# Performance work log

Hardware: AMD Instinct MI355X
Metric: run time of the kernel (lower is better)

The kernel has to match this reference:

```python
import jax, jax.numpy as jnp
import numpy as np

N = 50000        # nodes
E = 800000       # edges (avg degree 16)
DIN = 256        # input feature dim
D = 128          # embedding_dim
B = 8            # graphs in batch
ITERS = 2        # num_iterations


def setup_inputs() -> dict:
    key = jax.random.key(0)
    ks = jax.random.split(key, 16)
    w = lambda k, shape: jax.random.normal(k, shape, jnp.float32) * 0.05
    z = lambda n: jnp.zeros((n,), jnp.float32)
    return {
        "nodes": jax.random.normal(ks[0], (N, DIN), jnp.float32),
        "edges": jax.random.randint(ks[1], (2, E), 0, N),
        "batch": jnp.sort(jax.random.randint(ks[2], (N,), 0, B)),
        # initial encoder Linear(DIN, D)
        "W_enc": w(ks[3], (DIN, D)), "b_enc": z(D),
        # parent aggregation MLP: Linear(2D, D) -> ReLU -> Linear(D, D)
        "Wp1": w(ks[4], (2 * D, D)), "bp1": z(D),
        "Wp2": w(ks[5], (D, D)), "bp2": z(D),
        # child aggregation MLP
        "Wc1": w(ks[6], (2 * D, D)), "bc1": z(D),
        "Wc2": w(ks[7], (D, D)), "bc2": z(D),
        # final agg: Linear(3D, 2D) -> ReLU -> Linear(2D, D)
        "Wf1": w(ks[8], (3 * D, 2 * D)), "bf1": z(2 * D),
        "Wf2": w(ks[9], (2 * D, D)), "bf2": z(D),
        # Conv1d(D, 2D, kernel=1) == Linear(D, 2D)
        "Wconv": w(ks[10], (D, 2 * D)), "bconv": z(2 * D),
    }


def _edge_agg(x, idx_i, idx_j, W1, b1, W2, b2, inv_deg):
    # message: mlp(cat(x_i, x_j)); scatter-sum at idx_i; degree-normalize.
    h = jnp.concatenate([x[idx_i], x[idx_j]], axis=1)         # [E, 2D]
    m = jax.nn.relu(h @ W1 + b1) @ W2 + b2                    # [E, D]
    agg = jax.ops.segment_sum(m, idx_i, num_segments=x.shape[0])
    return agg * inv_deg[:, None]


def reference(nodes, edges, batch, W_enc, b_enc, Wp1, bp1, Wp2, bp2,
              Wc1, bc1, Wc2, bc2, Wf1, bf1, Wf2, bf2, Wconv, bconv):
    src, dst = edges[0], edges[1]
    ones_e = jnp.ones((edges.shape[1],), nodes.dtype)
    deg_dst = jax.ops.segment_sum(ones_e, dst, num_segments=N)
    deg_src = jax.ops.segment_sum(ones_e, src, num_segments=N)
    inv_dst = jnp.where(deg_dst > 0, 1.0 / deg_dst, 0.0)
    inv_src = jnp.where(deg_src > 0, 1.0 / deg_src, 0.0)

    x = nodes @ W_enc + b_enc                                  # [N, D]
    for _ in range(ITERS):
        # Parent_Aggregation: x_i = x[dst], x_j = x[src], sum at dst, / in-deg
        fi = _edge_agg(x, dst, src, Wp1, bp1, Wp2, bp2, inv_dst)
        # Child_Aggregation:  x_i = x[src], x_j = x[dst], sum at src, / out-deg
        fo = _edge_agg(x, src, dst, Wc1, bc1, Wc2, bc2, inv_src)
        h = jnp.concatenate([x, fi, fo], axis=1)               # [N, 3D]
        x = x + (jax.nn.relu(h @ Wf1 + bf1) @ Wf2 + bf2)

    y = x @ Wconv + bconv                                      # conv1d k=1 -> [N, 2D]
    gmax = jax.ops.segment_max(y, batch, num_segments=B)       # global_max_pool
    cnt = jax.ops.segment_sum(jnp.ones((N,), y.dtype), batch, num_segments=B)
    gmean = jax.ops.segment_sum(y, batch, num_segments=B) / cnt[:, None]
    return jnp.concatenate([gmax, gmean], axis=1)              # [B, 4D]
```

## Files before the change

### kernel.cpp

```cpp
#include <hip/hip_runtime.h>
#include <hip/hip_bf16.h>
#include <float.h>

typedef __hip_bfloat16 bf16;
typedef short short8 __attribute__((ext_vector_type(8)));
typedef short short4v __attribute__((ext_vector_type(4)));
typedef float f32x4 __attribute__((ext_vector_type(4)));
typedef unsigned short u16;
typedef unsigned char u8;

__device__ __forceinline__ float toF(bf16 v) { return __bfloat162float(v); }
__device__ __forceinline__ float s2f(short s) {
    return __uint_as_float(((unsigned int)(unsigned short)s) << 16);
}
__device__ __forceinline__ short f2s(float f) {
    bf16 h = __float2bfloat16(f);
    return *(short*)&h;
}
__device__ __forceinline__ float rdw(const void* p, int i, int f) {
    return f ? toF(((const bf16*)p)[i]) : ((const float*)p)[i];
}

__global__ void diag_kernel(float* __restrict__ out, float v, int n) {
    int i = blockIdx.x * 256 + threadIdx.x;
    if (i < n) out[i] = v;
}

__global__ void init_kernel(int* __restrict__ deg2, float* __restrict__ cnt_gsum,
                            float* __restrict__ gmax, int* __restrict__ flag, int n2) {
    int i = blockIdx.x * 256 + threadIdx.x;
    if (i < n2) deg2[i] = 0;
    if (i < 8 + 2048) cnt_gsum[i] = 0.f;
    if (i < 2048) gmax[i] = -FLT_MAX;
    if (i == 0) *flag = 1;
}

__global__ void probe_kernel(const unsigned int* __restrict__ w, int nwords,
                             int* __restrict__ flag) {
    int i = blockIdx.x * 256 + threadIdx.x;
    bool bad = false;
    if (i < nwords) {
        float v = __uint_as_float((w[i] & 0xFFFFu) << 16);
        bad = !(v > -1e3f && v < 1e3f);
    }
    if (__any(bad) && (threadIdx.x & 63) == 0) atomicAnd(flag, 0);
}

struct M1 {
    const int* edges; int E;
    int* degd; int* degs; u8* rankd; u8* ranks;
    const int* batch; int Nn; float* cnt;
    const void* wsrc[7]; int woff[7]; bf16* wdst[7];
    int wK[7]; int wNC[7]; int wstart[8];
    const void* bsrc[8]; bf16* bdst[8]; int bn[8];
    const void* nsrc; bf16* ndst; int nElems;
    const void* w2praw; const void* w2craw; const void* wf1raw;
    const void* b2praw; const void* b2craw;
    bf16* wsf1; bf16* ub; bf16* vb;
    const int* flag;
    int sCnt, sSwz, sBias, sConv, sFw, sUv;
};

__global__ void mega1_kernel(M1 a) {
    int b = blockIdx.x, tid = threadIdx.x;
    if (b < a.sCnt) {
        const int* es = a.edges;
        const int* ed = a.edges + a.E;
        int e0 = (b * 256 + tid) * 4;
        if (e0 + 4 <= a.E) {
            int4 s4 = *(const int4*)(es + e0);
            int4 d4 = *(const int4*)(ed + e0);
            uchar4 rs, rd;
            rs.x = (u8)atomicAdd(&a.degs[s4.x], 1);
            rs.y = (u8)atomicAdd(&a.degs[s4.y], 1);
            rs.z = (u8)atomicAdd(&a.degs[s4.z], 1);
            rs.w = (u8)atomicAdd(&a.degs[s4.w], 1);
            rd.x = (u8)atomicAdd(&a.degd[d4.x], 1);
            rd.y = (u8)atomicAdd(&a.degd[d4.y], 1);
            rd.z = (u8)atomicAdd(&a.degd[d4.z], 1);
            rd.w = (u8)atomicAdd(&a.degd[d4.w], 1);
            *(uchar4*)(a.ranks + e0) = rs;
            *(uchar4*)(a.rankd + e0) = rd;
        } else {
            for (int e = e0; e < a.E; ++e) {
                a.ranks[e] = (u8)atomicAdd(&a.degs[es[e]], 1);
                a.rankd[e] = (u8)atomicAdd(&a.degd[ed[e]], 1);
            }
        }
    } else if (b < a.sSwz) {
        __shared__ float loc[8];
        if (tid < 8) loc[tid] = 0.f;
        __syncthreads();
        int i = (b - a.sCnt) * 256 + tid;
        if (i < a.Nn) atomicAdd(&loc[a.batch[i]], 1.0f);
        __syncthreads();
        if (tid < 8 && loc[tid] > 0.f) atomicAdd(&a.cnt[tid], loc[tid]);
    } else if (b < a.sBias) {
        int bb = b - a.sSwz;
        int seg = 0;
#pragma unroll
        for (int t = 1; t < 7; ++t) if (bb >= a.wstart[t]) seg = t;
        int i = (bb - a.wstart[seg]) * 256 + tid;
        int K = a.wK[seg], NC = a.wNC[seg];
        if (i < K * NC) {
            int KF = K >> 5;
            int j = i & 7;
            int ln = (i >> 3) & 63;
            int q = i >> 9;
            int kb = q % KF;
            int t = q / KF;
            int k = kb * 32 + (ln >> 4) * 8 + j;
            int n = t * 16 + (ln & 15);
            int idx = a.woff[seg] + k * NC + n;
            a.wdst[seg][i] = (*a.flag)
                ? ((const bf16*)a.wsrc[seg])[idx]
                : __float2bfloat16(((const float*)a.wsrc[seg])[idx]);
        }
    } else if (b < a.sConv) {
#pragma unroll
        for (int t = 0; t < 8; ++t)
            for (int i = tid; i < a.bn[t]; i += 256)
                a.bdst[t][i] = (*a.flag)
                    ? ((const bf16*)a.bsrc[t])[i]
                    : __float2bfloat16(((const float*)a.bsrc[t])[i]);
    } else if (b < a.sFw) {
        if (*a.flag) return;
        int i = (b - a.sConv) * 2048 + tid * 8;
        if (i + 8 <= a.nElems) {
            const float* f = (const float*)a.nsrc + i;
            short8 o;
#pragma unroll
            for (int j = 0; j < 8; ++j) o[j] = f2s(f[j]);
            *(short8*)((short*)a.ndst + i) = o;
        } else {
            int e = a.nElems;
            for (int jj = i; jj < e && jj < i + 8; ++jj)
                a.ndst[jj] = __float2bfloat16(((const float*)a.nsrc)[jj]);
        }
    } else if (b < a.sUv) {
        int i = (b - a.sFw) * 256 + tid;
        int j = i & 7;
        int ln = (i >> 3) & 63;
        int q = i >> 9;
        int kb = q % 12;
        int t = q / 12;
        int k = kb * 32 + (ln >> 4) * 8 + j;
        int n = t * 16 + (ln & 15);
        int f = *a.flag;
        float val;
        if (k < 128) {
            val = rdw(a.wf1raw, k * 256 + n, f);
        } else {
            const void* w2 = (k < 256) ? a.w2praw : a.w2craw;
            int arow = k & 127;
            int base = (k < 256) ? 128 : 256;
            float s = 0.f;
            for (int c = 0; c < 128; ++c)
                s += rdw(w2, arow * 128 + c, f) * rdw(a.wf1raw, (base + c) * 256 + n, f);
            val = s;
        }
        a.wsf1[i] = __float2bfloat16(val);
    } else {
        if (tid < 256) {
            int f = *a.flag;
            float su = 0.f, sv = 0.f;
            for (int c = 0; c < 128; ++c) {
                su += rdw(a.b2praw, c, f) * rdw(a.wf1raw, (128 + c) * 256 + tid, f);
                sv += rdw(a.b2craw, c, f) * rdw(a.wf1raw, (256 + c) * 256 + tid, f);
            }
            a.ub[tid] = __float2bfloat16(su);
            a.vb[tid] = __float2bfloat16(sv);
        }
    }
}

__device__ __forceinline__ void atomicMaxF(float* addr, float val) {
    unsigned int* ua = (unsigned int*)addr;
    unsigned int old = __float_as_uint(*addr);
    while (__uint_as_float(old) < val) {
        unsigned int assumed = old;
        old = atomicCAS(ua, assumed, __float_as_uint(val));
        if (old == assumed) break;
    }
}

template<int K, int NC> struct SB {
    static constexpr int APAD = K + 8;
    static constexpr int CPAD = NC + 8;
    static constexpr int AB = 64 * APAD * 2;
    static constexpr int CB = 64 * CPAD * 2;
    static constexpr int S = AB > CB ? AB : CB;
};

template<int K, int NC, int NSRC, bool RELU, bool RES, bool POOL, bool STORE>
__device__ __forceinline__ void gemm_core(int bx,
    const bf16* A0, const bf16* A1, const bf16* A2,
    const bf16* WS, const bf16* bias, bf16* C, int M,
    const int* batch, float* gmax, float* gsum, char* smem) {
    constexpr int KF = K / 32;
    constexpr int NH = NC / 128;
    constexpr int APAD = SB<K, NC>::APAD;
    constexpr int CPAD = SB<K, NC>::CPAD;
    short* sA = (short*)smem;

    int tid = threadIdx.x;
    int m0blk = bx * 64;

    constexpr int C8 = K / 8;
    for (int idx = tid; idx < 64 * C8; idx += 256) {
        int r = idx / C8, c8 = idx % C8;
        int row = m0blk + r; row = row < M ? row : M - 1;
        const bf16* src;
        int off;
        if (NSRC == 1) { src = A0; off = c8 * 8; }
        else {
            int seg = c8 >> 4;
            src = seg == 0 ? A0 : (seg == 1 ? A1 : A2);
            off = (c8 & 15) * 8;
        }
        const size_t rs = (NSRC == 1) ? (size_t)K : (size_t)128;
        *(short8*)(sA + r * APAD + c8 * 8) = *(const short8*)((const short*)src + (size_t)row * rs + off);
    }
    __syncthreads();

    int wv = tid >> 6, ln = tid & 63;
    int quad = ln >> 4, ncol = ln & 15;
    int mw = wv * 16;

    short8 a[KF];
#pragma unroll
    for (int kb = 0; kb < KF; ++kb)
        a[kb] = *(const short8*)(sA + (mw + ncol) * APAD + kb * 32 + quad * 8);
    __syncthreads();

    short* sC = (short*)smem;
    const short8* wsp = (const short8*)WS;
#pragma unroll
    for (int h = 0; h < NH; ++h) {
        f32x4 acc[8];
#pragma unroll
        for (int t = 0; t < 8; ++t) acc[t] = (f32x4){0.f, 0.f, 0.f, 0.f};
        short8 bcur[8], bnxt[8];
#pragma unroll
        for (int t = 0; t < 8; ++t)
            bcur[t] = wsp[(size_t)((h * 8 + t) * KF) * 64 + ln];
#pragma unroll
        for (int kb = 0; kb < KF; ++kb) {
            if (kb + 1 < KF) {
#pragma unroll
                for (int t = 0; t < 8; ++t)
                    bnxt[t] = wsp[(size_t)((h * 8 + t) * KF + kb + 1) * 64 + ln];
            }
#pragma unroll
            for (int t = 0; t < 8; ++t)
                acc[t] = __builtin_amdgcn_mfma_f32_16x16x32_bf16(a[kb], bcur[t], acc[t], 0, 0, 0);
#pragma unroll
            for (int t = 0; t < 8; ++t) bcur[t] = bnxt[t];
        }
#pragma unroll
        for (int t = 0; t < 8; ++t) {
            float bv = bias ? toF(bias[h * 128 + t * 16 + ncol]) : 0.f;
#pragma unroll
            for (int r = 0; r < 4; ++r) {
                float v = acc[t][r] + bv;
                if (RELU) v = fmaxf(v, 0.f);
                sC[(mw + quad * 4 + r) * CPAD + h * 128 + t * 16 + ncol] = f2s(v);
            }
        }
    }
    __syncthreads();
    if (!STORE && !POOL) return;

    if (POOL) {
        int* bs = (int*)(smem + SB<K, NC>::S);
        if (tid < 64) {
            int row = m0blk + tid;
            bs[tid] = (row < M) ? batch[row] : -1;
        }
        __syncthreads();
        int cur_b = -1;
        float mx = -FLT_MAX, sm = 0.f;
        for (int r = 0; r < 64; ++r) {
            int b = bs[r];
            if (b < 0) break;
            float v = s2f(sC[r * CPAD + tid]);
            if (b != cur_b) {
                if (cur_b >= 0) {
                    atomicMaxF(&gmax[cur_b * 256 + tid], mx);
                    atomicAdd(&gsum[cur_b * 256 + tid], sm);
                }
                cur_b = b; mx = v; sm = v;
            } else {
                mx = fmaxf(mx, v);
                sm += v;
            }
        }
        if (cur_b >= 0) {
            atomicMaxF(&gmax[cur_b * 256 + tid], mx);
            atomicAdd(&gsum[cur_b * 256 + tid], sm);
        }
    } else {
        constexpr int OC8 = NC / 8;
        for (int idx = tid; idx < 64 * OC8; idx += 256) {
            int r = idx / OC8, c8 = idx % OC8;
            int row = m0blk + r;
            if (row < M) {
                short8 v = *(short8*)(sC + r * CPAD + c8 * 8);
                size_t o = (size_t)row * NC + c8 * 8;
                if (RES) {
                    short8 old = *(const short8*)((const short*)C + o);
#pragma unroll
                    for (int j = 0; j < 8; ++j) v[j] = f2s(s2f(v[j]) + s2f(old[j]));
                }
                *(short8*)((short*)C + o) = v;
            }
        }
    }
}

template<int K, int NC, int NSRC, bool RELU, bool RES, bool POOL>
__global__ __launch_bounds__(256, 2)
void gemm_mfma_kernel(const bf16* A0, const bf16* A1, const bf16* A2,
                      const bf16* WS, const bf16* bias, bf16* C, int M,
                      const int* batch, float* gmax, float* gsum) {
    __shared__ __align__(16) char smem[SB<K, NC>::S + (POOL ? 256 : 0)];
    gemm_core<K, NC, NSRC, RELU, RES, POOL, true>(
        blockIdx.x, A0, A1, A2, WS, bias, C, M, batch, gmax, gsum, smem);
}

__global__ __launch_bounds__(256, 2)
void sei_kernel(const int* __restrict__ edges, int E,
                const u8* __restrict__ rankd, const u8* __restrict__ ranks,
                u16* __restrict__ adjd, u16* __restrict__ adjs, int CAP,
                const void* nodes_raw, const bf16* Tn, const int* flag,
                const bf16* WSenc, const bf16* benc, bf16* x, int M,
                const int* degd, const int* degs,
                float* invd, float* invs, int gsc, int gb) {
    __shared__ __align__(16) char smem[SB<256, 128>::S];
    int b = blockIdx.x, tid = threadIdx.x;
    if (b < gsc) {
        int e0 = (b * 256 + tid) * 4;
        if (e0 + 4 <= E) {
            int4 s4 = *(const int4*)(edges + e0);
            int4 d4 = *(const int4*)(edges + E + e0);
            uchar4 rs = *(const uchar4*)(ranks + e0);
            uchar4 rd = *(const uchar4*)(rankd + e0);
            if (rs.x < CAP) adjs[s4.x * CAP + rs.x] = (u16)d4.x;
            if (rs.y < CAP) adjs[s4.y * CAP + rs.y] = (u16)d4.y;
            if (rs.z < CAP) adjs[s4.z * CAP + rs.z] = (u16)d4.z;
            if (rs.w < CAP) adjs[s4.w * CAP + rs.w] = (u16)d4.w;
            if (rd.x < CAP) adjd[d4.x * CAP + rd.x] = (u16)s4.x;
            if (rd.y < CAP) adjd[d4.y * CAP + rd.y] = (u16)s4.y;
            if (rd.z < CAP) adjd[d4.z * CAP + rd.z] = (u16)s4.z;
            if (rd.w < CAP) adjd[d4.w * CAP + rd.w] = (u16)s4.w;
        } else {
            for (int e = e0; e < E; ++e) {
                int s_ = edges[e], d_ = edges[E + e];
                if (ranks[e] < CAP) adjs[s_ * CAP + ranks[e]] = (u16)d_;
                if (rankd[e] < CAP) adjd[d_ * CAP + rankd[e]] = (u16)s_;
            }
        }
    } else if (b < gsc + gb) {
        const bf16* A0 = (*flag) ? (const bf16*)nodes_raw : Tn;
        gemm_core<256, 128, 1, false, false, false, true>(
            b - gsc, A0, nullptr, nullptr, WSenc, benc, x, M,
            nullptr, nullptr, nullptr, smem);
    } else {
        int i = (b - gsc - gb) * 256 + tid;
        if (i < M) {
            int dd = degd[i]; invd[i] = dd > 0 ? 1.0f / (float)dd : 0.0f;
            int ds = degs[i]; invs[i] = ds > 0 ? 1.0f / (float)ds : 0.0f;
        }
    }
}

__device__ __forceinline__ void agg_body(int node, int tid,
        const int* __restrict__ deg, const u16* __restrict__ adj, int CAP,
        const float* __restrict__ inv,
        const short* __restrict__ PQ, int stride,
        const short* __restrict__ b1, bf16* __restrict__ S) {
    int ln = tid & 63;
    int c4 = ln & 31, half = ln >> 5;
    float p[4];
    {
        short4v pv = *(const short4v*)(PQ + (size_t)node * stride + 4 * c4);
        short4v bv = *(const short4v*)(b1 + 4 * c4);
#pragma unroll
        for (int r = 0; r < 4; ++r) p[r] = s2f(pv[r]) + s2f(bv[r]);
    }
    float a[4] = {0.f, 0.f, 0.f, 0.f};
    int d = deg[node]; d = d < CAP ? d : CAP;
    float invv = inv[node];
    const u16* ap = adj + (size_t)node * CAP;
    const short* Qb = PQ + 128 + 4 * c4;
    int k = half;
    for (; k + 14 < d; k += 16) {
        int j0 = ap[k],      j1 = ap[k + 2],  j2 = ap[k + 4],  j3 = ap[k + 6];
        int j4 = ap[k + 8],  j5 = ap[k + 10], j6 = ap[k + 12], j7 = ap[k + 14];
        short4v q0 = *(const short4v*)(Qb + (size_t)j0 * stride);
        short4v q1 = *(const short4v*)(Qb + (size_t)j1 * stride);
        short4v q2 = *(const short4v*)(Qb + (size_t)j2 * stride);
        short4v q3 = *(const short4v*)(Qb + (size_t)j3 * stride);
        short4v q4 = *(const short4v*)(Qb + (size_t)j4 * stride);
        short4v q5 = *(const short4v*)(Qb + (size_t)j5 * stride);
        short4v q6 = *(const short4v*)(Qb + (size_t)j6 * stride);
        short4v q7 = *(const short4v*)(Qb + (size_t)j7 * stride);
#pragma unroll
        for (int r = 0; r < 4; ++r)
            a[r] += fmaxf(p[r] + s2f(q0[r]), 0.f) + fmaxf(p[r] + s2f(q1[r]), 0.f)
                  + fmaxf(p[r] + s2f(q2[r]), 0.f) + fmaxf(p[r] + s2f(q3[r]), 0.f)
                  + fmaxf(p[r] + s2f(q4[r]), 0.f) + fmaxf(p[r] + s2f(q5[r]), 0.f)
                  + fmaxf(p[r] + s2f(q6[r]), 0.f) + fmaxf(p[r] + s2f(q7[r]), 0.f);
    }
    for (; k + 6 < d; k += 8) {
        int j0 = ap[k], j1 = ap[k + 2], j2 = ap[k + 4], j3 = ap[k + 6];
        short4v q0 = *(const short4v*)(Qb + (size_t)j0 * stride);
        short4v q1 = *(const short4v*)(Qb + (size_t)j1 * stride);
        short4v q2 = *(const short4v*)(Qb + (size_t)j2 * stride);
        short4v q3 = *(const short4v*)(Qb + (size_t)j3 * stride);
#pragma unroll
        for (int r = 0; r < 4; ++r)
            a[r] += fmaxf(p[r] + s2f(q0[r]), 0.f) + fmaxf(p[r] + s2f(q1[r]), 0.f)
                  + fmaxf(p[r] + s2f(q2[r]), 0.f) + fmaxf(p[r] + s2f(q3[r]), 0.f);
    }
    for (; k < d; k += 2) {
        int j = ap[k];
        short4v q = *(const short4v*)(Qb + (size_t)j * stride);
#pragma unroll
        for (int r = 0; r < 4; ++r) a[r] += fmaxf(p[r] + s2f(q[r]), 0.f);
    }
#pragma unroll
    for (int r = 0; r < 4; ++r) a[r] += __shfl_xor(a[r], 32);
    if (half == 0) {
        short4v o;
#pragma unroll
        for (int r = 0; r < 4; ++r) o[r] = f2s(a[r] * invv);
        *(short4v*)((short*)S + (size_t)node * 128 + 4 * c4) = o;
    }
}

__global__ void agg_kernel(const int* deg, const u16* adj, int CAP,
                           const float* inv, const bf16* PQ, int stride,
                           const bf16* b1, bf16* S, int M) {
    int node = blockIdx.x * 4 + (threadIdx.x >> 6);
    if (node >= M) return;
    agg_body(node, threadIdx.x, deg, adj, CAP, inv, (const short*)PQ, stride,
             (const short*)b1, S);
}

__global__ void agg2_kernel(const int* degd, const u16* adjd, const float* invd,
                            const int* degs, const u16* adjs, const float* invs,
                            int CAP, const bf16* T, const bf16* b1p, const bf16* b1c,
                            bf16* Sd, bf16* Ss, int M, int ga) {
    int b = blockIdx.x, wv = threadIdx.x >> 6;
    if (b < ga) {
        int node = b * 4 + wv;
        if (node < M)
            agg_body(node, threadIdx.x, degd, adjd, CAP, invd, (const short*)T, 512,
                     (const short*)b1p, Sd);
    } else {
        int node = (b - ga) * 4 + wv;
        if (node < M)
            agg_body(node, threadIdx.x, degs, adjs, CAP, invs, (const short*)T + 256, 512,
                     (const short*)b1c, Ss);
    }
}

template<bool FINAL>
__global__ __launch_bounds__(256, 2)
void mega_mlp_kernel(const bf16* __restrict__ x, const bf16* Sd, const bf16* Ss,
                     const int* __restrict__ degd, const int* __restrict__ degs,
                     const bf16* __restrict__ ub, const bf16* __restrict__ vb,
                     const bf16* WSf1, const bf16* bf1_,
                     const bf16* WSf2, const bf16* bf2_,
                     bf16* xio, int M,
                     const bf16* WSconv, const bf16* bconv,
                     const int* batch, float* gmax, float* gsum) {
    __shared__ __align__(16) char smem[52224 + 256];
    constexpr int RB = 17408;
    short* sm = (short*)smem;
    int tid = threadIdx.x;
    int m0blk = blockIdx.x * 64;

#pragma unroll
    for (int reg = 0; reg < 3; ++reg) {
        const short* sp = reg == 0 ? (const short*)x
                        : (reg == 1 ? (const short*)Sd : (const short*)Ss);
        for (int idx = tid; idx < 64 * 16; idx += 256) {
            int r = idx >> 4, c8 = idx & 15;
            int row = m0blk + r; row = row < M ? row : M - 1;
            *(short8*)(sm + reg * (RB / 2) + r * 136 + c8 * 8) =
                *(const short8*)(sp + (size_t)row * 128 + c8 * 8);
        }
    }
    __syncthreads();

    int wv = tid >> 6, ln = tid & 63;
    int quad = ln >> 4, ncol = ln & 15;
    int mw = wv * 16;

    short8 a1[12];
#pragma unroll
    for (int kb = 0; kb < 12; ++kb) {
        const short* sb = sm + (kb >> 2) * (RB / 2);
        a1[kb] = *(const short8*)(sb + (mw + ncol) * 136 + (kb & 3) * 32 + quad * 8);
    }
    __syncthreads();

    bool md[4], ms[4];
#pragma unroll
    for (int r = 0; r < 4; ++r) {
        int orow = m0blk + mw + quad * 4 + r; orow = orow < M ? orow : M - 1;
        md[r] = degd[orow] > 0;
        ms[r] = degs[orow] > 0;
    }

    short* sH = sm + RB / 2;
    const short8* w1 = (const short8*)WSf1;
#pragma unroll
    for (int h = 0; h < 2; ++h) {
        f32x4 acc[8];
#pragma unroll
        for (int t = 0; t < 8; ++t) acc[t] = (f32x4){0.f, 0.f, 0.f, 0.f};
        short8 bcur[8], bnxt[8];
#pragma unroll
        for (int t = 0; t < 8; ++t)
            bcur[t] = w1[(size_t)((h * 8 + t) * 12) * 64 + ln];
#pragma unroll
        for (int kb = 0; kb < 12; ++kb) {
            if (kb + 1 < 12) {
#pragma unroll
                for (int t = 0; t < 8; ++t)
                    bnxt[t] = w1[(size_t)((h * 8 + t) * 12 + kb + 1) * 64 + ln];
            }
#pragma unroll
            for (int t = 0; t < 8; ++t)
                acc[t] = __builtin_amdgcn_mfma_f32_16x16x32_bf16(a1[kb], bcur[t], acc[t], 0, 0, 0);
#pragma unroll
            for (int t = 0; t < 8; ++t) bcur[t] = bnxt[t];
        }
#pragma unroll
        for (int t = 0; t < 8; ++t) {
            int col = h * 128 + t * 16 + ncol;
            float bv = toF(bf1_[col]);
            float uu = toF(ub[col]);
            float vv = toF(vb[col]);
#pragma unroll
            for (int r = 0; r < 4; ++r) {
                float v = acc[t][r] + bv + (md[r] ? uu : 0.f) + (ms[r] ? vv : 0.f);
                sH[(mw + quad * 4 + r) * 264 + col] = f2s(fmaxf(v, 0.f));
            }
        }
    }
    __syncthreads();

    short8 a2[8];
#pragma unroll
    for (int kb = 0; kb < 8; ++kb)
        a2[kb] = *(const short8*)(sH + (mw + ncol) * 264 + kb * 32 + quad * 8);
    __syncthreads();

    f32x4 acc2[8];
#pragma unroll
    for (int t = 0; t < 8; ++t) acc2[t] = (f32x4){0.f, 0.f, 0.f, 0.f};
    const short8* w2 = (const short8*)WSf2;
    {
        short8 bcur[8], bnxt[8];
#pragma unroll
        for (int t = 0; t < 8; ++t) bcur[t] = w2[(size_t)(t * 8) * 64 + ln];
#pragma unroll
        for (int kb = 0; kb < 8; ++kb) {
            if (kb + 1 < 8) {
#pragma unroll
                for (int t = 0; t < 8; ++t)
                    bnxt[t] = w2[(size_t)(t * 8 + kb + 1) * 64 + ln];
            }
#pragma unroll
            for (int t = 0; t < 8; ++t)
                acc2[t] = __builtin_amdgcn_mfma_f32_16x16x32_bf16(a2[kb], bcur[t], acc2[t], 0, 0, 0);
#pragma unroll
            for (int t = 0; t < 8; ++t) bcur[t] = bnxt[t];
        }
    }
    short* sC2 = sm + RB / 2;
#pragma unroll
    for (int t = 0; t < 8; ++t) {
        float bv = toF(bf2_[t * 16 + ncol]);
#pragma unroll
        for (int r = 0; r < 4; ++r)
            sC2[(mw + quad * 4 + r) * 136 + t * 16 + ncol] = f2s(acc2[t][r] + bv);
    }
    __syncthreads();

    for (int idx = tid; idx < 64 * 16; idx += 256) {
        int r = idx >> 4, c8 = idx & 15;
        short8 v = *(short8*)(sC2 + r * 136 + c8 * 8);
        short8 old = *(const short8*)(sm + r * 136 + c8 * 8);
#pragma unroll
        for (int j = 0; j < 8; ++j) v[j] = f2s(s2f(v[j]) + s2f(old[j]));
        if (FINAL) {
            *(short8*)(sC2 + r * 136 + c8 * 8) = v;
        } else {
            int row = m0blk + r;
            if (row < M) *(short8*)((short*)xio + (size_t)row * 128 + c8 * 8) = v;
        }
    }
    if (!FINAL) return;
    __syncthreads();

    short8 a3[4];
#pragma unroll
    for (int kb = 0; kb < 4; ++kb)
        a3[kb] = *(const short8*)(sC2 + (mw + ncol) * 136 + kb * 32 + quad * 8);
    __syncthreads();

    short* sCc = sm;
    const short8* wc = (const short8*)WSconv;
#pragma unroll
    for (int h = 0; h < 2; ++h) {
        f32x4 acc[8];
#pragma unroll
        for (int t = 0; t < 8; ++t) acc[t] = (f32x4){0.f, 0.f, 0.f, 0.f};
        short8 bcur[8], bnxt[8];
#pragma unroll
        for (int t = 0; t < 8; ++t)
            bcur[t] = wc[(size_t)((h * 8 + t) * 4) * 64 + ln];
#pragma unroll
        for (int kb = 0; kb < 4; ++kb) {
            if (kb + 1 < 4) {
#pragma unroll
                for (int t = 0; t < 8; ++t)
                    bnxt[t] = wc[(size_t)((h * 8 + t) * 4 + kb + 1) * 64 + ln];
            }
#pragma unroll
            for (int t = 0; t < 8; ++t)
                acc[t] = __builtin_amdgcn_mfma_f32_16x16x32_bf16(a3[kb], bcur[t], acc[t], 0, 0, 0);
#pragma unroll
            for (int t = 0; t < 8; ++t) bcur[t] = bnxt[t];
        }
#pragma unroll
        for (int t = 0; t < 8; ++t) {
            float bv = toF(bconv[h * 128 + t * 16 + ncol]);
#pragma unroll
            for (int r = 0; r < 4; ++r)
                sCc[(mw + quad * 4 + r) * 264 + h * 128 + t * 16 + ncol] =
                    f2s(acc[t][r] + bv);
        }
    }
    __syncthreads();

    int* bs = (int*)(smem + 52224);
    if (tid < 64) {
        int row = m0blk + tid;
        bs[tid] = (row < M) ? batch[row] : -1;
    }
    __syncthreads();
    int cur_b = -1;
    float mx = -FLT_MAX, sum_ = 0.f;
    for (int r = 0; r < 64; ++r) {
        int b = bs[r];
        if (b < 0) break;
        float v = s2f(sCc[r * 264 + tid]);
        if (b != cur_b) {
            if (cur_b >= 0) {
                atomicMaxF(&gmax[cur_b * 256 + tid], mx);
                atomicAdd(&gsum[cur_b * 256 + tid], sum_);
            }
            cur_b = b; mx = v; sum_ = v;
        } else {
            mx = fmaxf(mx, v);
            sum_ += v;
        }
    }
    if (cur_b >= 0) {
        atomicMaxF(&gmax[cur_b * 256 + tid], mx);
        atomicAdd(&gsum[cur_b * 256 + tid], sum_);
    }
}

__global__ void out_kernel(const float* __restrict__ gmax, const float* __restrict__ gsum,
                           const float* __restrict__ cnt, const int* __restrict__ flag,
                           void* __restrict__ out) {
    int i = blockIdx.x * 256 + threadIdx.x;
    if (i < 8 * 512) {
        int b = i >> 9, c = i & 511;
        float v = (c < 256) ? gmax[b * 256 + c] : gsum[b * 256 + (c - 256)] / cnt[b];
        int f = *flag;
        if (!(v == v)) v = 1000.f + 100.f * (float)f;
        if (f) ((bf16*)out)[i] = __float2bfloat16(v);
        else   ((float*)out)[i] = v;
    }
}

extern "C" void kernel_launch(void* const* d_in, const int* in_sizes, int n_in,
                              void* d_out, int out_size, void* d_ws, size_t ws_size,
                              hipStream_t stream) {
    const int* edges = (const int*)d_in[1];
    const int* batch = (const int*)d_in[2];

    const int N_ = in_sizes[2];
    const int E_ = in_sizes[1] / 2;
    const size_t ND = (size_t)N_ * 128;

    char* p = (char*)d_ws;
    bf16* x  = (bf16*)p;      p += ND * 2;
    bf16* Sd = (bf16*)p;      p += ND * 2;
    bf16* Ss = (bf16*)p;      p += ND * 2;
    bf16* bias[8];
    for (int t = 0; t < 8; ++t) { bias[t] = (bf16*)p; p += 512 * 2; }
    bf16* ub      = (bf16*)p; p += 256 * 2;
    bf16* vb      = (bf16*)p; p += 256 * 2;
    bf16* WSenc   = (bf16*)p; p += 256 * 128 * 2;
    bf16* WSpqall = (bf16*)p; p += 4 * 128 * 128 * 2;
    bf16* WSf1    = (bf16*)p; p += 384 * 256 * 2;
    bf16* WSf2    = (bf16*)p; p += 256 * 128 * 2;
    bf16* WSconv  = (bf16*)p; p += 128 * 256 * 2;
    int* degd    = (int*)p;   p += (size_t)N_ * 4;
    int* degs    = (int*)p;   p += (size_t)N_ * 4;
    float* invd  = (float*)p; p += (size_t)N_ * 4;
    float* invs  = (float*)p; p += (size_t)N_ * 4;
    float* cnt   = (float*)p; p += 8 * 4;
    float* gsum  = (float*)p; p += 2048 * 4;
    float* gmax  = (float*)p; p += 2048 * 4;
    int* flag    = (int*)p;   p += 64;
    u8* rankd    = (u8*)p;    p += ((size_t)E_ + 15) & ~(size_t)15;
    u8* ranks    = (u8*)p;    p += ((size_t)E_ + 15) & ~(size_t)15;

    size_t used = (size_t)(p - (char*)d_ws);
    size_t rem = ws_size > used ? ws_size - used : 0;
    int CAP = 0, wide = 0;
    if (N_ < 65536) {
        if      (rem >= (size_t)2 * N_ * 64 * 2 + (size_t)N_ * 512 * 2) { CAP = 64; wide = 1; }
        else if (rem >= (size_t)2 * N_ * 64 * 2 + (size_t)N_ * 256 * 2) { CAP = 64; wide = 0; }
        else if (rem >= (size_t)2 * N_ * 48 * 2 + (size_t)N_ * 256 * 2) { CAP = 48; wide = 0; }
    }
    if (!CAP) {
        diag_kernel<<<(out_size + 255) / 256, 256, 0, stream>>>((float*)d_out, (float)(ws_size >> 20), out_size);
        return;
    }
    u16* adjd = (u16*)p;      p += (size_t)N_ * CAP * 2;
    u16* adjs = (u16*)p;      p += (size_t)N_ * CAP * 2;
    bf16* T   = (bf16*)p;

    int gN  = (N_ + 255) / 256;
    int gE4 = (E_ + 1023) / 1024;
    int gb  = (N_ + 63) / 64;
    int ga  = (N_ + 3) / 4;

    init_kernel<<<(2 * N_ + 255) / 256, 256, 0, stream>>>(degd, cnt, gmax, flag, 2 * N_);
    probe_kernel<<<8, 256, 0, stream>>>((const unsigned int*)d_in[3], 2048, flag);

    M1 a;
    a.edges = edges; a.E = E_;
    a.degd = degd; a.degs = degs; a.rankd = rankd; a.ranks = ranks;
    a.batch = batch; a.Nn = N_; a.cnt = cnt;
    a.nsrc = d_in[0]; a.ndst = T; a.nElems = in_sizes[0];
    a.w2praw = d_in[7]; a.w2craw = d_in[11]; a.wf1raw = d_in[13];
    a.b2praw = d_in[8]; a.b2craw = d_in[12];
    a.wsf1 = WSf1; a.ub = ub; a.vb = vb;
    {
        const int bidx[8] = {4, 6, 8, 10, 12, 14, 16, 18};
        for (int t = 0; t < 8; ++t) {
            a.bsrc[t] = d_in[bidx[t]];
            a.bdst[t] = bias[t];
            a.bn[t] = in_sizes[bidx[t]];
        }
        const void* wraw[7] = {d_in[3], d_in[5], d_in[5], d_in[9], d_in[9],
                               d_in[15], d_in[17]};
        int woff[7]  = {0, 0, 128 * 128, 0, 128 * 128, 0, 0};
        bf16* wdst[7] = {WSenc, WSpqall, WSpqall + 16384, WSpqall + 32768,
                         WSpqall + 49152, WSf2, WSconv};
        int wK[7]  = {256, 128, 128, 128, 128, 256, 128};
        int wNC[7] = {128, 128, 128, 128, 128, 128, 256};
        int wb_ = 0;
        for (int t = 0; t < 7; ++t) {
            a.wsrc[t] = wraw[t]; a.woff[t] = woff[t]; a.wdst[t] = wdst[t];
            a.wK[t] = wK[t]; a.wNC[t] = wNC[t];
            a.wstart[t] = wb_;
            wb_ += (wK[t] * wNC[t] + 255) / 256;
        }
        a.wstart[7] = wb_;
        a.flag = flag;
        a.sCnt  = gE4;
        a.sSwz  = a.sCnt + gN;
        a.sBias = a.sSwz + wb_;
        a.sConv = a.sBias + 1;
        int convB = (a.nElems + 2047) / 2048;
        a.sFw = a.sConv + convB;
        a.sUv = a.sFw + 384;
        mega1_kernel<<<a.sUv + 1, 256, 0, stream>>>(a);
    }

    sei_kernel<<<gE4 + gb + gN, 256, 0, stream>>>(
        edges, E_, rankd, ranks, adjd, adjs, CAP,
        d_in[0], T, flag, WSenc, bias[0], x, N_,
        degd, degs, invd, invs, gE4, gb);

    for (int it = 0; it < 2; ++it) {
        if (wide) {
            gemm_mfma_kernel<128, 512, 1, false, false, false><<<gb, 256, 0, stream>>>(
                x, nullptr, nullptr, WSpqall, nullptr, T, N_, nullptr, nullptr, nullptr);
            agg2_kernel<<<2 * ga, 256, 0, stream>>>(degd, adjd, invd, degs, adjs, invs,
                                                    CAP, T, bias[1], bias[3], Sd, Ss, N_, ga);
        } else {
            gemm_mfma_kernel<128, 256, 1, false, false, false><<<gb, 256, 0, stream>>>(
                x, nullptr, nullptr, WSpqall, nullptr, T, N_, nullptr, nullptr, nullptr);
            agg_kernel<<<ga, 256, 0, stream>>>(degd, adjd, CAP, invd, T, 256, bias[1], Sd, N_);
            gemm_mfma_kernel<128, 256, 1, false, false, false><<<gb, 256, 0, stream>>>(
                x, nullptr, nullptr, WSpqall + 32768, nullptr, T, N_, nullptr, nullptr, nullptr);
            agg_kernel<<<ga, 256, 0, stream>>>(degs, adjs, CAP, invs, T, 256, bias[3], Ss, N_);
        }
        if (it == 0)
            mega_mlp_kernel<false><<<gb, 256, 0, stream>>>(
                x, Sd, Ss, degd, degs, ub, vb,
                WSf1, bias[5], WSf2, bias[6], x, N_,
                WSconv, bias[7], batch, gmax, gsum);
        else
            mega_mlp_kernel<true><<<gb, 256, 0, stream>>>(
                x, Sd, Ss, degd, degs, ub, vb,
                WSf1, bias[5], WSf2, bias[6], x, N_,
                WSconv, bias[7], batch, gmax, gsum);
    }

    out_kernel<<<16, 256, 0, stream>>>(gmax, gsum, cnt, flag, d_out);
}
```

Before: 637.1 us.

## Fuse fp32 node conversion into encoder GEMM, fold bias, widen agg gathers

The separate fp32-to-bf16 conversion pass over the node features is removed. The encoder GEMM now reads fp32 directly and converts while loading its tile into shared memory. The folded Wf1 weight and bias precompute moves from the first mega kernel into sei_kernel blocks. The first-layer message bias is folded into the PQ GEMM through a padded bias vector, so the aggregation no longer adds it per node. The aggregation now gathers 16-byte short8 chunks with 16 lanes per row and 4 neighbour groups, adds a two-step shuffle reduction, and sets launch bounds; this trades fewer, wider loads against more shuffles and possible load imbalance.

New measurement: 632.3 us. No clear change (-0.8%).

```diff
diff --git a/kernel.cpp b/kernel.cpp
--- a/kernel.cpp
+++ b/kernel.cpp
@@ -53,12 +53,9 @@
     const void* wsrc[7]; int woff[7]; bf16* wdst[7];
     int wK[7]; int wNC[7]; int wstart[8];
     const void* bsrc[8]; bf16* bdst[8]; int bn[8];
-    const void* nsrc; bf16* ndst; int nElems;
-    const void* w2praw; const void* w2craw; const void* wf1raw;
-    const void* b2praw; const void* b2craw;
-    bf16* wsf1; bf16* ub; bf16* vb;
+    const void* b1praw; const void* b1craw; bf16* b1wide;
     const int* flag;
-    int sCnt, sSwz, sBias, sConv, sFw, sUv;
+    int sCnt, sSwz, sBias;
 };
 
 __global__ void mega1_kernel(M1 a) {
@@ -116,60 +113,18 @@
                 ? ((const bf16*)a.wsrc[seg])[idx]
                 : __float2bfloat16(((const float*)a.wsrc[seg])[idx]);
         }
-    } else if (b < a.sConv) {
+    } else {
+        int f = *a.flag;
 #pragma unroll
         for (int t = 0; t < 8; ++t)
             for (int i = tid; i < a.bn[t]; i += 256)
-                a.bdst[t][i] = (*a.flag)
-                    ? ((const bf16*)a.bsrc[t])[i]
-                    : __float2bfloat16(((const float*)a.bsrc[t])[i]);
-    } else if (b < a.sFw) {
-        if (*a.flag) return;
-        int i = (b - a.sConv) * 2048 + tid * 8;
-        if (i + 8 <= a.nElems) {
-            const float* f = (const float*)a.nsrc + i;
-            short8 o;
-#pragma unroll
-            for (int j = 0; j < 8; ++j) o[j] = f2s(f[j]);
-            *(short8*)((short*)a.ndst + i) = o;
-        } else {
-            int e = a.nElems;
-            for (int jj = i; jj < e && jj < i + 8; ++jj)
-                a.ndst[jj] = __float2bfloat16(((const float*)a.nsrc)[jj]);
-        }
-    } else if (b < a.sUv) {
-        int i = (b - a.sFw) * 256 + tid;
-        int j = i & 7;
-        int ln = (i >> 3) & 63;
-        int q = i >> 9;
-        int kb = q % 12;
-        int t = q / 12;
-        int k = kb * 32 + (ln >> 4) * 8 + j;
-        int n = t * 16 + (ln & 15);
-        int f = *a.flag;
-        float val;
-        if (k < 128) {
-            val = rdw(a.wf1raw, k * 256 + n, f);
-        } else {
-            const void* w2 = (k < 256) ? a.w2praw : a.w2craw;
-            int arow = k & 127;
-            int base = (k < 256) ? 128 : 256;
-            float s = 0.f;
-            for (int c = 0; c < 128; ++c)
-                s += rdw(w2, arow * 128 + c, f) * rdw(a.wf1raw, (base + c) * 256 + n, f);
-            val = s;
-        }
-        a.wsf1[i] = __float2bfloat16(val);
-    } else {
-        if (tid < 256) {
-            int f = *a.flag;
-            float su = 0.f, sv = 0.f;
-            for (int c = 0; c < 128; ++c) {
-                su += rdw(a.b2praw, c, f) * rdw(a.wf1raw, (128 + c) * 256 + tid, f);
-                sv += rdw(a.b2craw, c, f) * rdw(a.wf1raw, (256 + c) * 256 + tid, f);
-            }
-            a.ub[tid] = __float2bfloat16(su);
-            a.vb[tid] = __float2bfloat16(sv);
+                a.bdst[t][i] = f ? ((const bf16*)a.bsrc[t])[i]
+                                 : __float2bfloat16(((const float*)a.bsrc[t])[i]);
+        for (int i = tid; i < 512; i += 256) {
+            float v = 0.f;
+            if (i < 128) v = rdw(a.b1praw, i, f);
+            else if (i >= 256 && i < 384) v = rdw(a.b1craw, i - 256, f);
+            a.b1wide[i] = __float2bfloat16(v);
         }
     }
 }
@@ -192,7 +147,7 @@
     static constexpr int S = AB > CB ? AB : CB;
 };
 
-template<int K, int NC, int NSRC, bool RELU, bool RES, bool POOL, bool STORE>
+template<int K, int NC, int NSRC, int ADT, bool RELU, bool RES, bool POOL, bool STORE>
 __device__ __forceinline__ void gemm_core(int bx,
     const bf16* A0, const bf16* A1, const bf16* A2,
     const bf16* WS, const bf16* bias, bf16* C, int M,
@@ -219,7 +174,19 @@
             off = (c8 & 15) * 8;
         }
         const size_t rs = (NSRC == 1) ? (size_t)K : (size_t)128;
-        *(short8*)(sA + r * APAD + c8 * 8) = *(const short8*)((const short*)src + (size_t)row * rs + off);
+        if (ADT == 0) {
+            *(short8*)(sA + r * APAD + c8 * 8) =
+                *(const short8*)((const short*)src + (size_t)row * rs + off);
+        } else {
+            const float* fp = (const float*)src;
+            size_t base = (size_t)row * rs + off;
+            float4 v0 = *(const float4*)(fp + base);
+            float4 v1 = *(const float4*)(fp + base + 4);
+            short8 o;
+            o[0] = f2s(v0.x); o[1] = f2s(v0.y); o[2] = f2s(v0.z); o[3] = f2s(v0.w);
+            o[4] = f2s(v1.x); o[5] = f2s(v1.y); o[6] = f2s(v1.z); o[7] = f2s(v1.w);
+            *(short8*)(sA + r * APAD + c8 * 8) = o;
+        }
     }
     __syncthreads();
 
@@ -324,7 +291,7 @@
                       const bf16* WS, const bf16* bias, bf16* C, int M,
                       const int* batch, float* gmax, float* gsum) {
     __shared__ __align__(16) char smem[SB<K, NC>::S + (POOL ? 256 : 0)];
-    gemm_core<K, NC, NSRC, RELU, RES, POOL, true>(
+    gemm_core<K, NC, NSRC, 0, RELU, RES, POOL, true>(
         blockIdx.x, A0, A1, A2, WS, bias, C, M, batch, gmax, gsum, smem);
 }
 
@@ -332,14 +299,52 @@
 void sei_kernel(const int* __restrict__ edges, int E,
                 const u8* __restrict__ rankd, const u8* __restrict__ ranks,
                 u16* __restrict__ adjd, u16* __restrict__ adjs, int CAP,
-                const void* nodes_raw, const bf16* Tn, const int* flag,
+                const void* nodes_raw, const int* flag,
                 const bf16* WSenc, const bf16* benc, bf16* x, int M,
                 const int* degd, const int* degs,
-                float* invd, float* invs, int gsc, int gb) {
+                float* invd, float* invs,
+                const void* w2praw, const void* w2craw, const void* wf1raw,
+                const void* b2praw, const void* b2craw,
+                bf16* wsf1, bf16* ub, bf16* vb,
+                int gsc, int gb) {
     __shared__ __align__(16) char smem[SB<256, 128>::S];
     int b = blockIdx.x, tid = threadIdx.x;
-    if (b < gsc) {
-        int e0 = (b * 256 + tid) * 4;
+    if (b < 384) {
+        int i = b * 256 + tid;
+        int j = i & 7;
+        int ln2 = (i >> 3) & 63;
+        int q = i >> 9;
+        int kb = q % 12;
+        int t = q / 12;
+        int k = kb * 32 + (ln2 >> 4) * 8 + j;
+        int n = t * 16 + (ln2 & 15);
+        int f = *flag;
+        float val;
+        if (k < 128) {
+            val = rdw(wf1raw, k * 256 + n, f);
+        } else {
+            const void* w2 = (k < 256) ? w2praw : w2craw;
+            int arow = k & 127;
+            int base = (k < 256) ? 128 : 256;
+            float s = 0.f;
+            for (int c = 0; c < 128; ++c)
+                s += rdw(w2, arow * 128 + c, f) * rdw(wf1raw, (base + c) * 256 + n, f);
+            val = s;
+        }
+        wsf1[i] = __float2bfloat16(val);
+    } else if (b == 384) {
+        if (tid < 256) {
+            int f = *flag;
+            float su = 0.f, sv = 0.f;
+            for (int c = 0; c < 128; ++c) {
+                su += rdw(b2praw, c, f) * rdw(wf1raw, (128 + c) * 256 + tid, f);
+                sv += rdw(b2craw, c, f) * rdw(wf1raw, (256 + c) * 256 + tid, f);
+            }
+            ub[tid] = __float2bfloat16(su);
+            vb[tid] = __float2bfloat16(sv);
+        }
+    } else if (b < 385 + gsc) {
+        int e0 = ((b - 385) * 256 + tid) * 4;
         if (e0 + 4 <= E) {
             int4 s4 = *(const int4*)(edges + e0);
             int4 d4 = *(const int4*)(edges + E + e0);
@@ -360,13 +365,18 @@
                 if (rankd[e] < CAP) adjd[d_ * CAP + rankd[e]] = (u16)s_;
             }
         }
-    } else if (b < gsc + gb) {
-        const bf16* A0 = (*flag) ? (const bf16*)nodes_raw : Tn;
-        gemm_core<256, 128, 1, false, false, false, true>(
-            b - gsc, A0, nullptr, nullptr, WSenc, benc, x, M,
-            nullptr, nullptr, nullptr, smem);
+    } else if (b < 385 + gsc + gb) {
+        int bx = b - 385 - gsc;
+        if (*flag)
+            gemm_core<256, 128, 1, 0, false, false, false, true>(
+                bx, (const bf16*)nodes_raw, nullptr, nullptr, WSenc, benc, x, M,
+                nullptr, nullptr, nullptr, smem);
+        else
+            gemm_core<256, 128, 1, 1, false, false, false, true>(
+                bx, (const bf16*)nodes_raw, nullptr, nullptr, WSenc, benc, x, M,
+                nullptr, nullptr, nullptr, smem);
     } else {
-        int i = (b - gsc - gb) * 256 + tid;
+        int i = (b - 385 - gsc - gb) * 256 + tid;
         if (i < M) {
             int dd = degd[i]; invd[i] = dd > 0 ? 1.0f / (float)dd : 0.0f;
             int ds = degs[i]; invs[i] = ds > 0 ? 1.0f / (float)ds : 0.0f;
@@ -377,92 +387,91 @@
 __device__ __forceinline__ void agg_body(int node, int tid,
         const int* __restrict__ deg, const u16* __restrict__ adj, int CAP,
         const float* __restrict__ inv,
-        const short* __restrict__ PQ, int stride,
-        const short* __restrict__ b1, bf16* __restrict__ S) {
+        const short* __restrict__ PQ, int stride, bf16* __restrict__ S) {
     int ln = tid & 63;
-    int c4 = ln & 31, half = ln >> 5;
-    float p[4];
+    int g = ln >> 4, c8 = ln & 15;
+    float p[8];
     {
-        short4v pv = *(const short4v*)(PQ + (size_t)node * stride + 4 * c4);
-        short4v bv = *(const short4v*)(b1 + 4 * c4);
-#pragma unroll
-        for (int r = 0; r < 4; ++r) p[r] = s2f(pv[r]) + s2f(bv[r]);
-    }
-    float a[4] = {0.f, 0.f, 0.f, 0.f};
+        short8 pv = *(const short8*)(PQ + (size_t)node * stride + c8 * 8);
+#pragma unroll
+        for (int r = 0; r < 8; ++r) p[r] = s2f(pv[r]);
+    }
+    float a[8] = {0.f, 0.f, 0.f, 0.f, 0.f, 0.f, 0.f, 0.f};
     int d = deg[node]; d = d < CAP ? d : CAP;
     float invv = inv[node];
     const u16* ap = adj + (size_t)node * CAP;
-    const short* Qb = PQ + 128 + 4 * c4;
-    int k = half;
-    for (; k + 14 < d; k += 16) {
-        int j0 = ap[k],      j1 = ap[k + 2],  j2 = ap[k + 4],  j3 = ap[k + 6];
-        int j4 = ap[k + 8],  j5 = ap[k + 10], j6 = ap[k + 12], j7 = ap[k + 14];
-        short4v q0 = *(const short4v*)(Qb + (size_t)j0 * stride);
-        short4v q1 = *(const short4v*)(Qb + (size_t)j1 * stride);
-        short4v q2 = *(const short4v*)(Qb + (size_t)j2 * stride);
-        short4v q3 = *(const short4v*)(Qb + (size_t)j3 * stride);
-        short4v q4 = *(const short4v*)(Qb + (size_t)j4 * stride);
-        short4v q5 = *(const short4v*)(Qb + (size_t)j5 * stride);
-        short4v q6 = *(const short4v*)(Qb + (size_t)j6 * stride);
-        short4v q7 = *(const short4v*)(Qb + (size_t)j7 * stride);
-#pragma unroll
-        for (int r = 0; r < 4; ++r)
+    const short* Qb = PQ + 128 + c8 * 8;
+    int k = g;
+    for (; k + 28 < d; k += 32) {
+        int j0 = ap[k],      j1 = ap[k + 4],  j2 = ap[k + 8],  j3 = ap[k + 12];
+        int j4 = ap[k + 16], j5 = ap[k + 20], j6 = ap[k + 24], j7 = ap[k + 28];
+        short8 q0 = *(const short8*)(Qb + (size_t)j0 * stride);
+        short8 q1 = *(const short8*)(Qb + (size_t)j1 * stride);
+        short8 q2 = *(const short8*)(Qb + (size_t)j2 * stride);
+        short8 q3 = *(const short8*)(Qb + (size_t)j3 * stride);
+        short8 q4 = *(const short8*)(Qb + (size_t)j4 * stride);
+        short8 q5 = *(const short8*)(Qb + (size_t)j5 * stride);
+        short8 q6 = *(const short8*)(Qb + (size_t)j6 * stride);
+        short8 q7 = *(const short8*)(Qb + (size_t)j7 * stride);
+#pragma unroll
+        for (int r = 0; r < 8; ++r)
             a[r] += fmaxf(p[r] + s2f(q0[r]), 0.f) + fmaxf(p[r] + s2f(q1[r]), 0.f)
                   + fmaxf(p[r] + s2f(q2[r]), 0.f) + fmaxf(p[r] + s2f(q3[r]), 0.f)
                   + fmaxf(p[r] + s2f(q4[r]), 0.f) + fmaxf(p[r] + s2f(q5[r]), 0.f)
                   + fmaxf(p[r] + s2f(q6[r]), 0.f) + fmaxf(p[r] + s2f(q7[r]), 0.f);
     }
-    for (; k + 6 < d; k += 8) {
-        int j0 = ap[k], j1 = ap[k + 2], j2 = ap[k + 4], j3 = ap[k + 6];
-        short4v q0 = *(const short4v*)(Qb + (size_t)j0 * stride);
-        short4v q1 = *(const short4v*)(Qb + (size_t)j1 * stride);
-        short4v q2 = *(const short4v*)(Qb + (size_t)j2 * stride);
-        short4v q3 = *(const short4v*)(Qb + (size_t)j3 * stride);
-#pragma unroll
-        for (int r = 0; r < 4; ++r)
+    for (; k + 12 < d; k += 16) {
+        int j0 = ap[k], j1 = ap[k + 4], j2 = ap[k + 8], j3 = ap[k + 12];
+        short8 q0 = *(const short8*)(Qb + (size_t)j0 * stride);
+        short8 q1 = *(const short8*)(Qb + (size_t)j1 * stride);
+        short8 q2 = *(const short8*)(Qb + (size_t)j2 * stride);
+        short8 q3 = *(const short8*)(Qb + (size_t)j3 * stride);
+#pragma unroll
+        for (int r = 0; r < 8; ++r)
             a[r] += fmaxf(p[r] + s2f(q0[r]), 0.f) + fmaxf(p[r] + s2f(q1[r]), 0.f)
                   + fmaxf(p[r] + s2f(q2[r]), 0.f) + fmaxf(p[r] + s2f(q3[r]), 0.f);
     }
-    for (; k < d; k += 2) {
+    for (; k < d; k += 4) {
         int j = ap[k];
-        short4v q = *(const short4v*)(Qb + (size_t)j * stride);
-#pragma unroll
-        for (int r = 0; r < 4; ++r) a[r] += fmaxf(p[r] + s2f(q[r]), 0.f);
-    }
-#pragma unroll
-    for (int r = 0; r < 4; ++r) a[r] += __shfl_xor(a[r], 32);
-    if (half == 0) {
-        short4v o;
-#pragma unroll
-        for (int r = 0; r < 4; ++r) o[r] = f2s(a[r] * invv);
-        *(short4v*)((short*)S + (size_t)node * 128 + 4 * c4) = o;
-    }
-}
-
-__global__ void agg_kernel(const int* deg, const u16* adj, int CAP,
-                           const float* inv, const bf16* PQ, int stride,
-                           const bf16* b1, bf16* S, int M) {
+        short8 q = *(const short8*)(Qb + (size_t)j * stride);
+#pragma unroll
+        for (int r = 0; r < 8; ++r) a[r] += fmaxf(p[r] + s2f(q[r]), 0.f);
+    }
+#pragma unroll
+    for (int r = 0; r < 8; ++r) {
+        a[r] += __shfl_xor(a[r], 16);
+        a[r] += __shfl_xor(a[r], 32);
+    }
+    if (g == 0) {
+        short8 o;
+#pragma unroll
+        for (int r = 0; r < 8; ++r) o[r] = f2s(a[r] * invv);
+        *(short8*)((short*)S + (size_t)node * 128 + c8 * 8) = o;
+    }
+}
+
+__global__ __launch_bounds__(256, 4)
+void agg_kernel(const int* deg, const u16* adj, int CAP,
+                const float* inv, const bf16* PQ, int stride,
+                bf16* S, int M) {
     int node = blockIdx.x * 4 + (threadIdx.x >> 6);
     if (node >= M) return;
-    agg_body(node, threadIdx.x, deg, adj, CAP, inv, (const short*)PQ, stride,
-             (const short*)b1, S);
-}
-
-__global__ void agg2_kernel(const int* degd, const u16* adjd, const float* invd,
-                            const int* degs, const u16* adjs, const float* invs,
-                            int CAP, const bf16* T, const bf16* b1p, const bf16* b1c,
-                            bf16* Sd, bf16* Ss, int M, int ga) {
+    agg_body(node, threadIdx.x, deg, adj, CAP, inv, (const short*)PQ, stride, S);
+}
+
+__global__ __launch_bounds__(256, 4)
+void agg2_kernel(const int* degd, const u16* adjd, const float* invd,
+                 const int* degs, const u16* adjs, const float* invs,
+                 int CAP, const bf16* T, bf16* Sd, bf16* Ss, int M, int ga) {
     int b = blockIdx.x, wv = threadIdx.x >> 6;
     if (b < ga) {
         int node = b * 4 + wv;
         if (node < M)
-            agg_body(node, threadIdx.x, degd, adjd, CAP, invd, (const short*)T, 512,
-                     (const short*)b1p, Sd);
+            agg_body(node, threadIdx.x, degd, adjd, CAP, invd, (const short*)T, 512, Sd);
     } else {
         int node = (b - ga) * 4 + wv;
         if (node < M)
-            agg_body(node, threadIdx.x, degs, adjs, CAP, invs, (const short*)T + 256, 512,
-                     (const short*)b1c, Ss);
+            agg_body(node, threadIdx.x, degs, adjs, CAP, invs, (const short*)T + 256, 512, Ss);
     }
 }
 
@@ -710,6 +719,7 @@
     for (int t = 0; t < 8; ++t) { bias[t] = (bf16*)p; p += 512 * 2; }
     bf16* ub      = (bf16*)p; p += 256 * 2;
     bf16* vb      = (bf16*)p; p += 256 * 2;
+    bf16* b1wide  = (bf16*)p; p += 512 * 2;
     bf16* WSenc   = (bf16*)p; p += 256 * 128 * 2;
     bf16* WSpqall = (bf16*)p; p += 4 * 128 * 128 * 2;
     bf16* WSf1    = (bf16*)p; p += 384 * 256 * 2;
@@ -754,10 +764,7 @@
     a.edges = edges; a.E = E_;
     a.degd = degd; a.degs = degs; a.rankd = rankd; a.ranks = ranks;
     a.batch = batch; a.Nn = N_; a.cnt = cnt;
-    a.nsrc = d_in[0]; a.ndst = T; a.nElems = in_sizes[0];
-    a.w2praw = d_in[7]; a.w2craw = d_in[11]; a.wf1raw = d_in[13];
-    a.b2praw = d_in[8]; a.b2craw = d_in[12];
-    a.wsf1 = WSf1; a.ub = ub; a.vb = vb;
+    a.b1praw = d_in[6]; a.b1craw = d_in[10]; a.b1wide = b1wide;
     {
         const int bidx[8] = {4, 6, 8, 10, 12, 14, 16, 18};
         for (int t = 0; t < 8; ++t) {
@@ -784,31 +791,29 @@
         a.sCnt  = gE4;
         a.sSwz  = a.sCnt + gN;
         a.sBias = a.sSwz + wb_;
-        a.sConv = a.sBias + 1;
-        int convB = (a.nElems + 2047) / 2048;
-        a.sFw = a.sConv + convB;
-        a.sUv = a.sFw + 384;
-        mega1_kernel<<<a.sUv + 1, 256, 0, stream>>>(a);
-    }
-
-    sei_kernel<<<gE4 + gb + gN, 256, 0, stream>>>(
+        mega1_kernel<<<a.sBias + 1, 256, 0, stream>>>(a);
+    }
+
+    sei_kernel<<<385 + gE4 + gb + gN, 256, 0, stream>>>(
         edges, E_, rankd, ranks, adjd, adjs, CAP,
-        d_in[0], T, flag, WSenc, bias[0], x, N_,
-        degd, degs, invd, invs, gE4, gb);
+        d_in[0], flag, WSenc, bias[0], x, N_,
+        degd, degs, invd, invs,
+        d_in[7], d_in[11], d_in[13], d_in[8], d_in[12],
+        WSf1, ub, vb, gE4, gb);
 
     for (int it = 0; it < 2; ++it) {
         if (wide) {
             gemm_mfma_kernel<128, 512, 1, false, false, false><<<gb, 256, 0, stream>>>(
-                x, nullptr, nullptr, WSpqall, nullptr, T, N_, nullptr, nullptr, nullptr);
+                x, nullptr, nullptr, WSpqall, b1wide, T, N_, nullptr, nullptr, nullptr);
             agg2_kernel<<<2 * ga, 256, 0, stream>>>(degd, adjd, invd, degs, adjs, invs,
-                                                    CAP, T, bias[1], bias[3], Sd, Ss, N_, ga);
+                                                    CAP, T, Sd, Ss, N_, ga);
         } else {
             gemm_mfma_kernel<128, 256, 1, false, false, false><<<gb, 256, 0, stream>>>(
-                x, nullptr, nullptr, WSpqall, nullptr, T, N_, nullptr, nullptr, nullptr);
-            agg_kernel<<<ga, 256, 0, stream>>>(degd, adjd, CAP, invd, T, 256, bias[1], Sd, N_);
+                x, nullptr, nullptr, WSpqall, b1wide, T, N_, nullptr, nullptr, nullptr);
+            agg_kernel<<<ga, 256, 0, stream>>>(degd, adjd, CAP, invd, T, 256, Sd, N_);
             gemm_mfma_kernel<128, 256, 1, false, false, false><<<gb, 256, 0, stream>>>(
-                x, nullptr, nullptr, WSpqall + 32768, nullptr, T, N_, nullptr, nullptr, nullptr);
-            agg_kernel<<<ga, 256, 0, stream>>>(degs, adjs, CAP, invs, T, 256, bias[3], Ss, N_);
+                x, nullptr, nullptr, WSpqall + 32768, b1wide + 256, T, N_, nullptr, nullptr, nullptr);
+            agg_kernel<<<ga, 256, 0, stream>>>(degs, adjs, CAP, invs, T, 256, Ss, N_);
         }
         if (it == 0)
             mega_mlp_kernel<false><<<gb, 256, 0, stream>>>(
```
